# Performance work log

Measured on AMD Instinct MI355X. Metric: run time of the kernel, lower is better.

The kernel has to match this reference:

```python
import jax, jax.numpy as jnp
import numpy as np

NUM_HEADS = 16
NUM_GROUPS = 4
HIDDEN = 2048
HEAD_DIM = HIDDEN // NUM_HEADS  # 128


def setup_inputs() -> dict:
    key = jax.random.key(0)
    ks = jax.random.split(key, 9)
    B, S = 2, 2048
    kv_dim = NUM_GROUPS * HEAD_DIM
    sc_in = 1.0 / np.sqrt(HIDDEN)
    return {
        "X": jax.random.normal(ks[0], (B, S, HIDDEN), dtype=jnp.float32),
        "Wq": jax.random.normal(ks[1], (HIDDEN, HIDDEN), dtype=jnp.float32) * sc_in,
        "bq": jnp.zeros((HIDDEN,), jnp.float32),
        "Wk": jax.random.normal(ks[2], (kv_dim, HIDDEN), dtype=jnp.float32) * sc_in,
        "bk": jnp.zeros((kv_dim,), jnp.float32),
        "Wv": jax.random.normal(ks[3], (kv_dim, HIDDEN), dtype=jnp.float32) * sc_in,
        "bv": jnp.zeros((kv_dim,), jnp.float32),
        "Wo": jax.random.normal(ks[4], (HIDDEN, HIDDEN), dtype=jnp.float32) * sc_in,
        "bo": jnp.zeros((HIDDEN,), jnp.float32),
    }


def reference(X, Wq, bq, Wk, bk, Wv, bv, Wo, bo):
    B, S, D = X.shape
    H, G, hd = NUM_HEADS, NUM_GROUPS, HEAD_DIM
    rep = H // G

    q = X @ Wq.T + bq                          # (B,S,D)
    k = X @ Wk.T + bk                          # (B,S,G*hd)
    v = X @ Wv.T + bv                          # (B,S,G*hd)

    q = q.reshape(B, S, H, hd).transpose(0, 2, 1, 3)   # (B,H,S,hd)
    k = k.reshape(B, S, G, hd).transpose(0, 2, 1, 3)   # (B,G,S,hd)
    v = v.reshape(B, S, G, hd).transpose(0, 2, 1, 3)
    # GQA head expansion: each kv group serves rep query heads
    k = jnp.repeat(k, rep, axis=1)             # (B,H,S,hd)
    v = jnp.repeat(v, rep, axis=1)

    scale = 1.0 / jnp.sqrt(jnp.asarray(hd, X.dtype))
    scores = jnp.einsum('bhqd,bhkd->bhqk', q, k) * scale  # (B,H,S,S)
    attn = jax.nn.softmax(scores, axis=-1)
    mid = jnp.einsum('bhqk,bhkd->bhqd', attn, v)          # (B,H,S,hd)
    mid = mid.transpose(0, 2, 1, 3).reshape(B, S, D)
    return mid @ Wo.T + bo
```

## Files before the change

### kernel.cpp

```cpp
#include <hip/hip_runtime.h>

using uint = unsigned int;
using ushort = unsigned short;

typedef float f32x4 __attribute__((ext_vector_type(4)));
typedef float f32x16 __attribute__((ext_vector_type(16)));
typedef uint u32x4 __attribute__((ext_vector_type(4)));
using short8 = __attribute__((ext_vector_type(8))) short;

__device__ __forceinline__ ushort f2bf(float f) {
  uint u = __float_as_uint(f);
  u += 0x7fffu + ((u >> 16) & 1u);
  return (ushort)(u >> 16);
}

#define GLOAD_LDS16(gptr, lptr)                                                   \
  __builtin_amdgcn_global_load_lds(                                               \
      (const __attribute__((address_space(1))) void*)(gptr),                      \
      (__attribute__((address_space(3))) void*)(lptr), 16, 0, 0)

__global__ void cast_f32_to_bf16(const float* __restrict__ in,
                                 ushort* __restrict__ out, int n4) {
  int stride = gridDim.x * blockDim.x;
  for (int i = blockIdx.x * blockDim.x + threadIdx.x; i < n4; i += stride) {
    float4 v = reinterpret_cast<const float4*>(in)[i];
    ushort4 o;
    o.x = f2bf(v.x); o.y = f2bf(v.y); o.z = f2bf(v.z); o.w = f2bf(v.w);
    reinterpret_cast<ushort4*>(out)[i] = o;
  }
}

__device__ __forceinline__ void gemm128_mainloop(const ushort* __restrict__ A,
                                                 const ushort* __restrict__ W,
                                                 int K, ushort* As, ushort* Bs,
                                                 f32x4 (&acc)[4][4]) {
  const int tid = threadIdx.x;
  const int lane = tid & 63;
  const int wr = (tid >> 7) & 1;
  const int wc = (tid >> 6) & 1;
  const char* aP = (const char*)(A + (size_t)(tid >> 2) * K) + (tid & 3) * 16;
  const char* bP = (const char*)(W + (size_t)(tid >> 2) * K) + (tid & 3) * 16;
  const size_t rowHop = (size_t)64 * K * 2;
  ushort* aL0 = As + tid * 8;
  ushort* aL1 = As + 2048 + tid * 8;
  ushort* bL0 = Bs + tid * 8;
  ushort* bL1 = Bs + 2048 + tid * 8;
  const int ar = lane & 15;
  const int ak = (lane >> 4) * 8;

  for (int k0 = 0; k0 < K; k0 += 32) {
    GLOAD_LDS16(aP, aL0);
    GLOAD_LDS16(aP + rowHop, aL1);
    GLOAD_LDS16(bP, bL0);
    GLOAD_LDS16(bP + rowHop, bL1);
    aP += 64; bP += 64;
    __syncthreads();
    short8 af[4], bf[4];
#pragma unroll
    for (int i = 0; i < 4; ++i)
      af[i] = *reinterpret_cast<const short8*>(&As[(wr * 64 + i * 16 + ar) * 32 + ak]);
#pragma unroll
    for (int i = 0; i < 4; ++i)
      bf[i] = *reinterpret_cast<const short8*>(&Bs[(wc * 64 + i * 16 + ar) * 32 + ak]);
#pragma unroll
    for (int mi = 0; mi < 4; ++mi)
#pragma unroll
      for (int ni = 0; ni < 4; ++ni)
        acc[mi][ni] = __builtin_amdgcn_mfma_f32_16x16x32_bf16(af[mi], bf[ni],
                                                              acc[mi][ni], 0, 0, 0);
    __syncthreads();
  }
}

__global__ __launch_bounds__(256) void qkv_gemm(
    const ushort* __restrict__ Xb, const ushort* __restrict__ Wq,
    const ushort* __restrict__ Wk, const ushort* __restrict__ Wv,
    const float* __restrict__ bq, const float* __restrict__ bk,
    const float* __restrict__ bv, ushort* __restrict__ Qb,
    ushort* __restrict__ Kb, ushort* __restrict__ Vt) {
  __shared__ ushort As[128 * 32], Bs[128 * 32];
  const int bx = blockIdx.x, by = blockIdx.y;
  const ushort* W; const float* bias; ushort* out;
  int n0, mode, ldo;
  if (bx < 16)      { W = Wq; bias = bq; out = Qb; n0 = bx * 128;        mode = 0; ldo = 2048; }
  else if (bx < 20) { W = Wk; bias = bk; out = Kb; n0 = (bx - 16) * 128; mode = 0; ldo = 512; }
  else              { W = Wv; bias = bv; out = Vt; n0 = (bx - 20) * 128; mode = 1; ldo = 0; }

  f32x4 acc[4][4] = {};
  gemm128_mainloop(Xb + (size_t)by * 128 * 2048, W + (size_t)n0 * 2048, 2048, As, Bs, acc);

  const int lane = threadIdx.x & 63;
  const int wr = (threadIdx.x >> 7) & 1, wc = (threadIdx.x >> 6) & 1;
  const int r0 = by * 128 + wr * 64 + ((lane >> 4) * 4);
  const int c0 = wc * 64 + (lane & 15);
#pragma unroll
  for (int mi = 0; mi < 4; ++mi)
#pragma unroll
    for (int ni = 0; ni < 4; ++ni) {
      const int col = c0 + ni * 16;
      const float bb = bias[n0 + col];
#pragma unroll
      for (int j = 0; j < 4; ++j) {
        const int row = r0 + mi * 16 + j;
        const float v = acc[mi][ni][j] + bb;
        if (mode == 0) {
          out[(size_t)row * ldo + n0 + col] = f2bf(v);
        } else {
          const int b = row >> 11, s = row & 2047;
          out[((size_t)(b * 512 + n0 + col) << 11) + s] = f2bf(v);
        }
      }
    }
}

__global__ __launch_bounds__(256) void out_gemm(const ushort* __restrict__ Mid,
                                                const ushort* __restrict__ Wo,
                                                const float* __restrict__ bo,
                                                float* __restrict__ Out) {
  __shared__ ushort As[128 * 32], Bs[128 * 32];
  const int bx = blockIdx.x, by = blockIdx.y;
  f32x4 acc[4][4] = {};
  gemm128_mainloop(Mid + (size_t)by * 128 * 2048, Wo + (size_t)bx * 128 * 2048,
                   2048, As, Bs, acc);
  const int lane = threadIdx.x & 63;
  const int wr = (threadIdx.x >> 7) & 1, wc = (threadIdx.x >> 6) & 1;
  const int r0 = by * 128 + wr * 64 + ((lane >> 4) * 4);
  const int c0 = bx * 128 + wc * 64 + (lane & 15);
#pragma unroll
  for (int mi = 0; mi < 4; ++mi)
#pragma unroll
    for (int ni = 0; ni < 4; ++ni) {
      const int col = c0 + ni * 16;
      const float bb = bo[col];
#pragma unroll
      for (int j = 0; j < 4; ++j)
        Out[(size_t)(r0 + mi * 16 + j) * 2048 + col] = acc[mi][ni][j] + bb;
    }
}

__global__ __launch_bounds__(256, 2) void attn_fwd(const ushort* __restrict__ Q,
                                                   const ushort* __restrict__ Kb,
                                                   const ushort* __restrict__ Vt,
                                                   ushort* __restrict__ Mid) {
  __shared__ ushort Ks[2][64 * 128];
  __shared__ ushort Vs[2][128 * 64];

  const int tid = threadIdx.x, lane = tid & 63, wave = tid >> 6;
  const int h = blockIdx.y, b = blockIdx.z, g = h >> 2;
  const int q0w = blockIdx.x * 128 + wave * 32;
  const int lq = lane & 31, hi = lane >> 5;

  const char* kbase = (const char*)Kb + ((size_t)b * 2048 * 512 + g * 128) * 2;
  const char* vbase = (const char*)Vt + ((size_t)(b * 512 + g * 128) * 2048) * 2;
  int kRow[4], kOff[4], vRow[4], vOff[4];
#pragma unroll
  for (int i = 0; i < 4; ++i) {
    const int off = (i * 256 + tid) * 16;
    const int r = off >> 8, c = off & 255;
    kRow[i] = r; kOff[i] = c ^ ((r & 7) << 4);
    const int rv = off >> 7, cv = off & 127;
    vRow[i] = rv; vOff[i] = cv ^ ((rv & 7) << 4);
  }

#pragma unroll
  for (int i = 0; i < 4; ++i) {
    GLOAD_LDS16(kbase + (size_t)kRow[i] * 1024 + kOff[i],
                (char*)Ks[0] + (i * 256 + tid) * 16);
    GLOAD_LDS16(vbase + (size_t)vRow[i] * 4096 + vOff[i],
                (char*)Vs[0] + (i * 256 + tid) * 16);
  }

  short8 qf[8];
  {
    const ushort* qp = Q + (size_t)(b * 2048 + q0w + lq) * 2048 + h * 128 + hi * 8;
#pragma unroll
    for (int dblk = 0; dblk < 8; ++dblk)
      qf[dblk] = *reinterpret_cast<const short8*>(qp + dblk * 16);
  }

  float m_s = -3.0e38f, l_s = 0.f;
  f32x16 o[4] = {};
  const float sc2 = 0.08838834764831843f * 1.44269504088896340736f;

  __syncthreads();

  for (int t = 0; t < 32; ++t) {
    const int cur = t & 1;
    if (t < 31) {
      const int kv0 = (t + 1) * 64;
#pragma unroll
      for (int i = 0; i < 4; ++i) {
        GLOAD_LDS16(kbase + (size_t)(kv0 + kRow[i]) * 1024 + kOff[i],
                    (char*)Ks[cur ^ 1] + (i * 256 + tid) * 16);
        GLOAD_LDS16(vbase + (size_t)vRow[i] * 4096 + kv0 * 2 + vOff[i],
                    (char*)Vs[cur ^ 1] + (i * 256 + tid) * 16);
      }
    }

    const char* ksb = (const char*)Ks[cur];
    f32x16 st0 = {}, st1 = {};
    const int kcol = (32 * 0 + 16 * hi);
    const int ksw = (lq & 7) << 4;
    __builtin_amdgcn_s_setprio(1);
#pragma unroll
    for (int dblk = 0; dblk < 8; ++dblk) {
      const int cb = (dblk * 32 + 16 * hi) ^ ksw;
      short8 kf0 = *reinterpret_cast<const short8*>(ksb + lq * 256 + cb);
      short8 kf1 = *reinterpret_cast<const short8*>(ksb + (32 + lq) * 256 + cb);
      st0 = __builtin_amdgcn_mfma_f32_32x32x16_bf16(kf0, qf[dblk], st0, 0, 0, 0);
      st1 = __builtin_amdgcn_mfma_f32_32x32x16_bf16(kf1, qf[dblk], st1, 0, 0, 0);
    }
    __builtin_amdgcn_s_setprio(0);
    (void)kcol;

    float pm = fmaxf(st0[0], st0[1]);
#pragma unroll
    for (int r = 2; r < 16; ++r) pm = fmaxf(pm, st0[r]);
#pragma unroll
    for (int r = 0; r < 16; ++r) pm = fmaxf(pm, st1[r]);
    pm = fmaxf(pm, __shfl_xor(pm, 32, 64));
    const float msc = pm * sc2;

    if (__any(msc > m_s + 8.f)) {
      const float mnew = fmaxf(m_s, msc);
      const float alpha = exp2f(m_s - mnew);
      m_s = mnew;
      l_s *= alpha;
#pragma unroll
      for (int r = 0; r < 16; ++r) {
        const int qr = (r & 3) + 8 * (r >> 2) + 4 * hi;
        const float ar = __shfl(alpha, qr, 64);
#pragma unroll
        for (int dblk = 0; dblk < 4; ++dblk) o[dblk][r] *= ar;
      }
    }

    float rs = 0.f;
#pragma unroll
    for (int r = 0; r < 16; ++r) {
      st0[r] = exp2f(fmaf(st0[r], sc2, -m_s));
      rs += st0[r];
    }
#pragma unroll
    for (int r = 0; r < 16; ++r) {
      st1[r] = exp2f(fmaf(st1[r], sc2, -m_s));
      rs += st1[r];
    }
    rs += __shfl_xor(rs, 32, 64);
    l_s += rs;

    short8 pa[4];
#pragma unroll
    for (int half = 0; half < 2; ++half) {
      const f32x16 pt = half ? st1 : st0;
#pragma unroll
      for (int kk = 0; kk < 2; ++kk) {
        const int Rx = kk * 8;
        uint w0, w1, w2, w3;
#pragma unroll
        for (int s2 = 0; s2 < 2; ++s2) {
          const int s = s2 * 2;
          const float x0 = pt[Rx + s],     x1 = pt[Rx + s + 1];
          const float y0 = pt[Rx + 4 + s], y1 = pt[Rx + 4 + s + 1];
          uint x, y;
          asm("v_cvt_pk_bf16_f32 %0, %1, %2" : "=v"(x) : "v"(x0), "v"(x1));
          asm("v_cvt_pk_bf16_f32 %0, %1, %2" : "=v"(y) : "v"(y0), "v"(y1));
          auto sw = __builtin_amdgcn_permlane32_swap(x, y, false, false);
          if (s2 == 0) { w0 = sw[0]; w2 = sw[1]; }
          else         { w1 = sw[0]; w3 = sw[1]; }
        }
        u32x4 wv = {w0, w1, w2, w3};
        pa[half * 2 + kk] = __builtin_bit_cast(short8, wv);
      }
    }

    const char* vsb = (const char*)Vs[cur];
    __builtin_amdgcn_s_setprio(1);
#pragma unroll
    for (int dblk = 0; dblk < 4; ++dblk) {
      const int rv = dblk * 32 + lq;
      const int vsw = (rv & 7) << 4;
#pragma unroll
      for (int ks = 0; ks < 4; ++ks) {
        short8 vf = *reinterpret_cast<const short8*>(
            vsb + rv * 128 + ((ks * 32 + 16 * hi) ^ vsw));
        o[dblk] = __builtin_amdgcn_mfma_f32_32x32x16_bf16(pa[ks], vf, o[dblk], 0, 0, 0);
      }
    }
    __builtin_amdgcn_s_setprio(0);

    __syncthreads();
  }

  const float linv = 1.f / l_s;
#pragma unroll
  for (int r = 0; r < 16; ++r) {
    const int qr = (r & 3) + 8 * (r >> 2) + 4 * hi;
    const float lv = __shfl(linv, qr, 64);
    ushort* mp = Mid + (size_t)(b * 2048 + q0w + qr) * 2048 + h * 128 + lq;
#pragma unroll
    for (int dblk = 0; dblk < 4; ++dblk)
      mp[dblk * 32] = f2bf(o[dblk][r] * lv);
  }
}

extern "C" void kernel_launch(void* const* d_in, const int* in_sizes, int n_in,
                              void* d_out, int out_size, void* d_ws, size_t ws_size,
                              hipStream_t stream) {
  const float* X  = (const float*)d_in[0];
  const float* Wq = (const float*)d_in[1];
  const float* bq = (const float*)d_in[2];
  const float* Wk = (const float*)d_in[3];
  const float* bk = (const float*)d_in[4];
  const float* Wv = (const float*)d_in[5];
  const float* bv = (const float*)d_in[6];
  const float* Wo = (const float*)d_in[7];
  const float* bo = (const float*)d_in[8];
  float* Out = (float*)d_out;

  char* ws = (char*)d_ws;
  ushort* Xb   = (ushort*)(ws);
  ushort* Wqb  = (ushort*)(ws + 16777216);
  ushort* Wkb  = (ushort*)(ws + 25165824);
  ushort* Wvb  = (ushort*)(ws + 27262976);
  ushort* Wob  = (ushort*)(ws + 29360128);
  ushort* Qb   = (ushort*)(ws + 37748736);
  ushort* Kbuf = (ushort*)(ws + 54525952);
  ushort* Vtb  = (ushort*)(ws + 58720256);
  ushort* Midb = (ushort*)(ws + 62914560);

  auto cast = [&](const float* src, ushort* dst, int n) {
    int n4 = n >> 2;
    int blocks = (n4 + 255) >> 8;
    if (blocks > 2048) blocks = 2048;
    cast_f32_to_bf16<<<dim3(blocks), dim3(256), 0, stream>>>(src, dst, n4);
  };
  cast(X,  Xb,  8388608);
  cast(Wq, Wqb, 4194304);
  cast(Wk, Wkb, 1048576);
  cast(Wv, Wvb, 1048576);
  cast(Wo, Wob, 4194304);

  qkv_gemm<<<dim3(24, 32), 256, 0, stream>>>(Xb, Wqb, Wkb, Wvb, bq, bk, bv,
                                             Qb, Kbuf, Vtb);
  attn_fwd<<<dim3(16, 16, 2), 256, 0, stream>>>(Qb, Kbuf, Vtb, Midb);
  out_gemm<<<dim3(16, 32), 256, 0, stream>>>(Midb, Wob, bo, Out);
}
```

Baseline: 227.9 us.

## Rewrite projection GEMMs as 8-wave ping-pong pipelined kernels with swizzled LDS

Replaces the 128x128 single-buffered GEMM mainloop with a templated 512-thread kernel that uses 256-wide N tiles, K=64 steps, double-buffered LDS filled by direct global-to-LDS loads with an XOR swizzle, and interleaved prefetch/MFMA phases gated by barriers and priority hints. Block IDs are remapped for L2 locality in both QKV and output GEMMs. The attention kernel's max and sum reductions become tree reductions to shorten dependency chains. The aim is to hide memory latency and cut LDS bank conflicts, at the cost of larger LDS use and fewer blocks (192 QKV blocks may underfill the GPU).

```diff
diff --git a/kernel.cpp b/kernel.cpp
--- a/kernel.cpp
+++ b/kernel.cpp
@@ -18,6 +18,8 @@
   __builtin_amdgcn_global_load_lds(                                               \
       (const __attribute__((address_space(1))) void*)(gptr),                      \
       (__attribute__((address_space(3))) void*)(lptr), 16, 0, 0)
+
+__device__ __forceinline__ int swz(int o) { return o ^ (((o >> 7) & 7) << 4); }
 
 __global__ void cast_f32_to_bf16(const float* __restrict__ in,
                                  ushort* __restrict__ out, int n4) {
@@ -30,71 +32,170 @@
   }
 }
 
-__device__ __forceinline__ void gemm128_mainloop(const ushort* __restrict__ A,
-                                                 const ushort* __restrict__ W,
-                                                 int K, ushort* As, ushort* Bs,
-                                                 f32x4 (&acc)[4][4]) {
+template <int BM>
+__device__ __forceinline__ void gemm8p(const char* Ab, const char* Bb, int K,
+                                       char* lds, f32x4 (&acc)[BM / 32][4]) {
+  constexpr int MI = BM / 32;
+  constexpr int MH = MI / 2;
+  constexpr int ABYTES = BM * 128;
+  constexpr int BUFB = ABYTES + 32768;
+  constexpr int NAU = BM / 64;
+  constexpr int TL = NAU + 4;
+
   const int tid = threadIdx.x;
   const int lane = tid & 63;
-  const int wr = (tid >> 7) & 1;
-  const int wc = (tid >> 6) & 1;
-  const char* aP = (const char*)(A + (size_t)(tid >> 2) * K) + (tid & 3) * 16;
-  const char* bP = (const char*)(W + (size_t)(tid >> 2) * K) + (tid & 3) * 16;
-  const size_t rowHop = (size_t)64 * K * 2;
-  ushort* aL0 = As + tid * 8;
-  ushort* aL1 = As + 2048 + tid * 8;
-  ushort* bL0 = Bs + tid * 8;
-  ushort* bL1 = Bs + 2048 + tid * 8;
-  const int ar = lane & 15;
-  const int ak = (lane >> 4) * 8;
-
-  for (int k0 = 0; k0 < K; k0 += 32) {
-    GLOAD_LDS16(aP, aL0);
-    GLOAD_LDS16(aP + rowHop, aL1);
-    GLOAD_LDS16(bP, bL0);
-    GLOAD_LDS16(bP + rowHop, bL1);
-    aP += 64; bP += 64;
-    __syncthreads();
-    short8 af[4], bf[4];
-#pragma unroll
-    for (int i = 0; i < 4; ++i)
-      af[i] = *reinterpret_cast<const short8*>(&As[(wr * 64 + i * 16 + ar) * 32 + ak]);
-#pragma unroll
-    for (int i = 0; i < 4; ++i)
-      bf[i] = *reinterpret_cast<const short8*>(&Bs[(wc * 64 + i * 16 + ar) * 32 + ak]);
-#pragma unroll
-    for (int mi = 0; mi < 4; ++mi)
-#pragma unroll
-      for (int ni = 0; ni < 4; ++ni)
-        acc[mi][ni] = __builtin_amdgcn_mfma_f32_16x16x32_bf16(af[mi], bf[ni],
-                                                              acc[mi][ni], 0, 0, 0);
-    __syncthreads();
-  }
-}
-
-__global__ __launch_bounds__(256) void qkv_gemm(
+  const int wm = (tid >> 8) & 1;
+  const int wn = (tid >> 6) & 3;
+  const int lr = lane & 15, lgk = lane >> 4;
+  const size_t K2 = (size_t)K * 2;
+  const int nt = K >> 6;
+
+  const char* srcA[NAU];
+#pragma unroll
+  for (int u = 0; u < NAU; ++u) {
+    int d = u * 8192 + tid * 16, s = swz(d);
+    srcA[u] = Ab + (size_t)(s >> 7) * K2 + (s & 127);
+  }
+  const char* srcB[4];
+#pragma unroll
+  for (int u = 0; u < 4; ++u) {
+    int d = u * 8192 + tid * 16, s = swz(d);
+    srcB[u] = Bb + (size_t)(s >> 7) * K2 + (s & 127);
+  }
+  char* dstA = lds + tid * 16;
+  char* dstB = lds + ABYTES + tid * 16;
+
+  auto stA = [&](int buf, int u, int t) {
+    GLOAD_LDS16(srcA[u] + (size_t)t * 128, dstA + buf * BUFB + u * 8192);
+  };
+  auto stB = [&](int buf, int u, int t) {
+    GLOAD_LDS16(srcB[u] + (size_t)t * 128, dstB + buf * BUFB + u * 8192);
+  };
+  auto rdA = [&](int buf, int mi, int kk) -> short8 {
+    int o = (wm * (BM / 2) + mi * 16 + lr) * 128 + kk * 64 + lgk * 16;
+    return *reinterpret_cast<const short8*>(lds + buf * BUFB + swz(o));
+  };
+  auto rdB = [&](int buf, int ni, int kk) -> short8 {
+    int o = (wn * 64 + ni * 16 + lr) * 128 + kk * 64 + lgk * 16;
+    return *reinterpret_cast<const short8*>(lds + buf * BUFB + ABYTES + swz(o));
+  };
+
+#pragma unroll
+  for (int u = 0; u < NAU; ++u) stA(0, u, 0);
+#pragma unroll
+  for (int u = 0; u < 4; ++u) stB(0, u, 0);
+#pragma unroll
+  for (int u = 0; u < NAU; ++u) stA(1, u, 1);
+#pragma unroll
+  for (int u = 0; u < 4; ++u) stB(1, u, 1);
+  asm volatile("s_waitcnt vmcnt(%0)" ::"n"(TL) : "memory");
+  __builtin_amdgcn_s_barrier();
+
+  short8 af[MH][2], bf[4][2];
+
+  for (int t = 0; t < nt; ++t) {
+    const int c = t & 1;
+    const bool pf = (t + 2 < nt);
+
+#pragma unroll
+    for (int mi = 0; mi < MH; ++mi) { af[mi][0] = rdA(c, mi, 0); af[mi][1] = rdA(c, mi, 1); }
+#pragma unroll
+    for (int ni = 0; ni < 2; ++ni) { bf[ni][0] = rdB(c, ni, 0); bf[ni][1] = rdB(c, ni, 1); }
+    __builtin_amdgcn_s_barrier();
+    __builtin_amdgcn_s_setprio(1);
+#pragma unroll
+    for (int mi = 0; mi < MH; ++mi)
+#pragma unroll
+      for (int ni = 0; ni < 2; ++ni)
+#pragma unroll
+        for (int kk = 0; kk < 2; ++kk)
+          acc[mi][ni] = __builtin_amdgcn_mfma_f32_16x16x32_bf16(af[mi][kk], bf[ni][kk], acc[mi][ni], 0, 0, 0);
+    __builtin_amdgcn_s_setprio(0);
+    __builtin_amdgcn_s_barrier();
+
+#pragma unroll
+    for (int ni = 2; ni < 4; ++ni) { bf[ni][0] = rdB(c, ni, 0); bf[ni][1] = rdB(c, ni, 1); }
+    if (pf) {
+      if constexpr (BM == 256) { stA(c, 0, t + 2); stA(c, 2, t + 2); }
+    }
+    __builtin_amdgcn_s_barrier();
+    __builtin_amdgcn_s_setprio(1);
+#pragma unroll
+    for (int mi = 0; mi < MH; ++mi)
+#pragma unroll
+      for (int ni = 2; ni < 4; ++ni)
+#pragma unroll
+        for (int kk = 0; kk < 2; ++kk)
+          acc[mi][ni] = __builtin_amdgcn_mfma_f32_16x16x32_bf16(af[mi][kk], bf[ni][kk], acc[mi][ni], 0, 0, 0);
+    __builtin_amdgcn_s_setprio(0);
+    __builtin_amdgcn_s_barrier();
+
+#pragma unroll
+    for (int mi = 0; mi < MH; ++mi) { af[mi][0] = rdA(c, MH + mi, 0); af[mi][1] = rdA(c, MH + mi, 1); }
+    if (pf) {
+#pragma unroll
+      for (int u = 0; u < 4; ++u) stB(c, u, t + 2);
+    }
+    __builtin_amdgcn_s_barrier();
+    __builtin_amdgcn_s_setprio(1);
+#pragma unroll
+    for (int mi = 0; mi < MH; ++mi)
+#pragma unroll
+      for (int ni = 0; ni < 2; ++ni)
+#pragma unroll
+        for (int kk = 0; kk < 2; ++kk)
+          acc[MH + mi][ni] = __builtin_amdgcn_mfma_f32_16x16x32_bf16(af[mi][kk], bf[ni][kk], acc[MH + mi][ni], 0, 0, 0);
+    __builtin_amdgcn_s_setprio(0);
+    __builtin_amdgcn_s_barrier();
+
+    if (pf) {
+      if constexpr (BM == 256) { stA(c, 1, t + 2); stA(c, 3, t + 2); }
+      else                     { stA(c, 0, t + 2); stA(c, 1, t + 2); }
+    }
+    __builtin_amdgcn_s_setprio(1);
+#pragma unroll
+    for (int mi = 0; mi < MH; ++mi)
+#pragma unroll
+      for (int ni = 2; ni < 4; ++ni)
+#pragma unroll
+        for (int kk = 0; kk < 2; ++kk)
+          acc[MH + mi][ni] = __builtin_amdgcn_mfma_f32_16x16x32_bf16(af[mi][kk], bf[ni][kk], acc[MH + mi][ni], 0, 0, 0);
+    __builtin_amdgcn_s_setprio(0);
+    if (t + 1 < nt) {
+      if (pf) { asm volatile("s_waitcnt vmcnt(%0)" ::"n"(TL) : "memory"); }
+      else    { asm volatile("s_waitcnt vmcnt(0)" ::: "memory"); }
+      __builtin_amdgcn_s_barrier();
+    }
+  }
+}
+
+__global__ __launch_bounds__(512) void qkv_gemm8(
     const ushort* __restrict__ Xb, const ushort* __restrict__ Wq,
     const ushort* __restrict__ Wk, const ushort* __restrict__ Wv,
     const float* __restrict__ bq, const float* __restrict__ bk,
     const float* __restrict__ bv, ushort* __restrict__ Qb,
     ushort* __restrict__ Kb, ushort* __restrict__ Vt) {
-  __shared__ ushort As[128 * 32], Bs[128 * 32];
-  const int bx = blockIdx.x, by = blockIdx.y;
+  __shared__ char lds[2 * (256 * 128 + 32768)];
+  int id = blockIdx.x;
+  id = (id & 7) * 24 + (id >> 3);
+  const int bx = id % 12, by = id / 12;
+
   const ushort* W; const float* bias; ushort* out;
   int n0, mode, ldo;
-  if (bx < 16)      { W = Wq; bias = bq; out = Qb; n0 = bx * 128;        mode = 0; ldo = 2048; }
-  else if (bx < 20) { W = Wk; bias = bk; out = Kb; n0 = (bx - 16) * 128; mode = 0; ldo = 512; }
-  else              { W = Wv; bias = bv; out = Vt; n0 = (bx - 20) * 128; mode = 1; ldo = 0; }
-
-  f32x4 acc[4][4] = {};
-  gemm128_mainloop(Xb + (size_t)by * 128 * 2048, W + (size_t)n0 * 2048, 2048, As, Bs, acc);
+  if (bx < 8)       { W = Wq; bias = bq; out = Qb; n0 = bx * 256;        mode = 0; ldo = 2048; }
+  else if (bx < 10) { W = Wk; bias = bk; out = Kb; n0 = (bx - 8) * 256;  mode = 0; ldo = 512; }
+  else              { W = Wv; bias = bv; out = Vt; n0 = (bx - 10) * 256; mode = 1; ldo = 0; }
+
+  f32x4 acc[8][4] = {};
+  gemm8p<256>((const char*)(Xb + (size_t)by * 256 * 2048),
+              (const char*)(W + (size_t)n0 * 2048), 2048, lds, acc);
 
   const int lane = threadIdx.x & 63;
-  const int wr = (threadIdx.x >> 7) & 1, wc = (threadIdx.x >> 6) & 1;
-  const int r0 = by * 128 + wr * 64 + ((lane >> 4) * 4);
-  const int c0 = wc * 64 + (lane & 15);
-#pragma unroll
-  for (int mi = 0; mi < 4; ++mi)
+  const int wm = (threadIdx.x >> 8) & 1, wn = (threadIdx.x >> 6) & 3;
+  const int r0 = by * 256 + wm * 128 + (lane >> 4) * 4;
+  const int c0 = wn * 64 + (lane & 15);
+#pragma unroll
+  for (int mi = 0; mi < 8; ++mi)
 #pragma unroll
     for (int ni = 0; ni < 4; ++ni) {
       const int col = c0 + ni * 16;
@@ -113,19 +214,23 @@
     }
 }
 
-__global__ __launch_bounds__(256) void out_gemm(const ushort* __restrict__ Mid,
-                                                const ushort* __restrict__ Wo,
-                                                const float* __restrict__ bo,
-                                                float* __restrict__ Out) {
-  __shared__ ushort As[128 * 32], Bs[128 * 32];
-  const int bx = blockIdx.x, by = blockIdx.y;
+__global__ __launch_bounds__(512) void out_gemm8(const ushort* __restrict__ Mid,
+                                                 const ushort* __restrict__ Wo,
+                                                 const float* __restrict__ bo,
+                                                 float* __restrict__ Out) {
+  __shared__ char lds[2 * (128 * 128 + 32768)];
+  int id = blockIdx.x;
+  id = (id & 7) * 32 + (id >> 3);
+  const int bx = id % 8, by = id / 8;
+
   f32x4 acc[4][4] = {};
-  gemm128_mainloop(Mid + (size_t)by * 128 * 2048, Wo + (size_t)bx * 128 * 2048,
-                   2048, As, Bs, acc);
+  gemm8p<128>((const char*)(Mid + (size_t)by * 128 * 2048),
+              (const char*)(Wo + (size_t)bx * 256 * 2048), 2048, lds, acc);
+
   const int lane = threadIdx.x & 63;
-  const int wr = (threadIdx.x >> 7) & 1, wc = (threadIdx.x >> 6) & 1;
-  const int r0 = by * 128 + wr * 64 + ((lane >> 4) * 4);
-  const int c0 = bx * 128 + wc * 64 + (lane & 15);
+  const int wm = (threadIdx.x >> 8) & 1, wn = (threadIdx.x >> 6) & 3;
+  const int r0 = by * 128 + wm * 64 + (lane >> 4) * 4;
+  const int c0 = bx * 256 + wn * 64 + (lane & 15);
 #pragma unroll
   for (int mi = 0; mi < 4; ++mi)
 #pragma unroll
@@ -199,7 +304,6 @@
 
     const char* ksb = (const char*)Ks[cur];
     f32x16 st0 = {}, st1 = {};
-    const int kcol = (32 * 0 + 16 * hi);
     const int ksw = (lq & 7) << 4;
     __builtin_amdgcn_s_setprio(1);
 #pragma unroll
@@ -211,14 +315,15 @@
       st1 = __builtin_amdgcn_mfma_f32_32x32x16_bf16(kf1, qf[dblk], st1, 0, 0, 0);
     }
     __builtin_amdgcn_s_setprio(0);
-    (void)kcol;
-
-    float pm = fmaxf(st0[0], st0[1]);
-#pragma unroll
-    for (int r = 2; r < 16; ++r) pm = fmaxf(pm, st0[r]);
-#pragma unroll
-    for (int r = 0; r < 16; ++r) pm = fmaxf(pm, st1[r]);
-    pm = fmaxf(pm, __shfl_xor(pm, 32, 64));
+
+    float mx[16];
+#pragma unroll
+    for (int r = 0; r < 16; ++r) mx[r] = fmaxf(st0[r], st1[r]);
+#pragma unroll
+    for (int s = 8; s >= 1; s >>= 1)
+#pragma unroll
+      for (int r = 0; r < s; ++r) mx[r] = fmaxf(mx[r], mx[r + s]);
+    float pm = fmaxf(mx[0], __shfl_xor(mx[0], 32, 64));
     const float msc = pm * sc2;
 
     if (__any(msc > m_s + 8.f)) {
@@ -235,17 +340,18 @@
       }
     }
 
-    float rs = 0.f;
+    float sm[16];
 #pragma unroll
     for (int r = 0; r < 16; ++r) {
       st0[r] = exp2f(fmaf(st0[r], sc2, -m_s));
-      rs += st0[r];
-    }
-#pragma unroll
-    for (int r = 0; r < 16; ++r) {
       st1[r] = exp2f(fmaf(st1[r], sc2, -m_s));
-      rs += st1[r];
-    }
+      sm[r] = st0[r] + st1[r];
+    }
+#pragma unroll
+    for (int s = 8; s >= 1; s >>= 1)
+#pragma unroll
+      for (int r = 0; r < s; ++r) sm[r] += sm[r + s];
+    float rs = sm[0];
     rs += __shfl_xor(rs, 32, 64);
     l_s += rs;
 
@@ -341,8 +447,8 @@
   cast(Wv, Wvb, 1048576);
   cast(Wo, Wob, 4194304);
 
-  qkv_gemm<<<dim3(24, 32), 256, 0, stream>>>(Xb, Wqb, Wkb, Wvb, bq, bk, bv,
-                                             Qb, Kbuf, Vtb);
+  qkv_gemm8<<<dim3(192), dim3(512), 0, stream>>>(Xb, Wqb, Wkb, Wvb, bq, bk, bv,
+                                                 Qb, Kbuf, Vtb);
   attn_fwd<<<dim3(16, 16, 2), 256, 0, stream>>>(Qb, Kbuf, Vtb, Midb);
-  out_gemm<<<dim3(16, 32), 256, 0, stream>>>(Midb, Wob, bo, Out);
-}
+  out_gemm8<<<dim3(256), dim3(512), 0, stream>>>(Midb, Wob, bo, Out);
+}
```

After: 236.4 us. 3.7% more time.

## Process two 32-row query sets per wave to reuse K/V LDS fragments

Applied to the files above, without the earlier changes.

Each wave now handles 64 query rows as two independent 32-row sets, so every K and V fragment read from LDS feeds two MFMAs. The grid is halved to 8 query blocks of 256 rows, and launch bounds drop to one block per CU to leave room for the doubled accumulators. The K swizzle widens to 16 rows, and the softmax max/sum reductions become tree-shaped. The cost is more VGPR pressure, lower occupancy, and only 256 blocks, which may leave CUs underused.

```diff
diff --git a/kernel.cpp b/kernel.cpp
--- a/kernel.cpp
+++ b/kernel.cpp
@@ -138,7 +138,7 @@
     }
 }
 
-__global__ __launch_bounds__(256, 2) void attn_fwd(const ushort* __restrict__ Q,
+__global__ __launch_bounds__(256, 1) void attn_fwd(const ushort* __restrict__ Q,
                                                    const ushort* __restrict__ Kb,
                                                    const ushort* __restrict__ Vt,
                                                    ushort* __restrict__ Mid) {
@@ -147,7 +147,7 @@
 
   const int tid = threadIdx.x, lane = tid & 63, wave = tid >> 6;
   const int h = blockIdx.y, b = blockIdx.z, g = h >> 2;
-  const int q0w = blockIdx.x * 128 + wave * 32;
+  const int q0w = blockIdx.x * 256 + wave * 64;
   const int lq = lane & 31, hi = lane >> 5;
 
   const char* kbase = (const char*)Kb + ((size_t)b * 2048 * 512 + g * 128) * 2;
@@ -157,7 +157,7 @@
   for (int i = 0; i < 4; ++i) {
     const int off = (i * 256 + tid) * 16;
     const int r = off >> 8, c = off & 255;
-    kRow[i] = r; kOff[i] = c ^ ((r & 7) << 4);
+    kRow[i] = r; kOff[i] = c ^ ((r & 15) << 4);
     const int rv = off >> 7, cv = off & 127;
     vRow[i] = rv; vOff[i] = cv ^ ((rv & 7) << 4);
   }
@@ -170,19 +170,24 @@
                 (char*)Vs[0] + (i * 256 + tid) * 16);
   }
 
-  short8 qf[8];
-  {
-    const ushort* qp = Q + (size_t)(b * 2048 + q0w + lq) * 2048 + h * 128 + hi * 8;
+  short8 qf[2][8];
+#pragma unroll
+  for (int set = 0; set < 2; ++set) {
+    const ushort* qp =
+        Q + (size_t)(b * 2048 + q0w + set * 32 + lq) * 2048 + h * 128 + hi * 8;
 #pragma unroll
     for (int dblk = 0; dblk < 8; ++dblk)
-      qf[dblk] = *reinterpret_cast<const short8*>(qp + dblk * 16);
-  }
-
-  float m_s = -3.0e38f, l_s = 0.f;
-  f32x16 o[4] = {};
+      qf[set][dblk] = *reinterpret_cast<const short8*>(qp + dblk * 16);
+  }
+
+  float m_s[2] = {-3.0e38f, -3.0e38f}, l_s[2] = {0.f, 0.f};
+  f32x16 o[2][4] = {};
   const float sc2 = 0.08838834764831843f * 1.44269504088896340736f;
 
   __syncthreads();
+
+  const int ksw = (lq & 15) << 4;
+  const int vsw = (lq & 7) << 4;
 
   for (int t = 0; t < 32; ++t) {
     const int cur = t & 1;
@@ -198,79 +203,87 @@
     }
 
     const char* ksb = (const char*)Ks[cur];
-    f32x16 st0 = {}, st1 = {};
-    const int kcol = (32 * 0 + 16 * hi);
-    const int ksw = (lq & 7) << 4;
+    f32x16 st[2][2] = {};
     __builtin_amdgcn_s_setprio(1);
 #pragma unroll
     for (int dblk = 0; dblk < 8; ++dblk) {
       const int cb = (dblk * 32 + 16 * hi) ^ ksw;
       short8 kf0 = *reinterpret_cast<const short8*>(ksb + lq * 256 + cb);
       short8 kf1 = *reinterpret_cast<const short8*>(ksb + (32 + lq) * 256 + cb);
-      st0 = __builtin_amdgcn_mfma_f32_32x32x16_bf16(kf0, qf[dblk], st0, 0, 0, 0);
-      st1 = __builtin_amdgcn_mfma_f32_32x32x16_bf16(kf1, qf[dblk], st1, 0, 0, 0);
+      st[0][0] = __builtin_amdgcn_mfma_f32_32x32x16_bf16(kf0, qf[0][dblk], st[0][0], 0, 0, 0);
+      st[0][1] = __builtin_amdgcn_mfma_f32_32x32x16_bf16(kf1, qf[0][dblk], st[0][1], 0, 0, 0);
+      st[1][0] = __builtin_amdgcn_mfma_f32_32x32x16_bf16(kf0, qf[1][dblk], st[1][0], 0, 0, 0);
+      st[1][1] = __builtin_amdgcn_mfma_f32_32x32x16_bf16(kf1, qf[1][dblk], st[1][1], 0, 0, 0);
     }
     __builtin_amdgcn_s_setprio(0);
-    (void)kcol;
-
-    float pm = fmaxf(st0[0], st0[1]);
-#pragma unroll
-    for (int r = 2; r < 16; ++r) pm = fmaxf(pm, st0[r]);
-#pragma unroll
-    for (int r = 0; r < 16; ++r) pm = fmaxf(pm, st1[r]);
-    pm = fmaxf(pm, __shfl_xor(pm, 32, 64));
-    const float msc = pm * sc2;
-
-    if (__any(msc > m_s + 8.f)) {
-      const float mnew = fmaxf(m_s, msc);
-      const float alpha = exp2f(m_s - mnew);
-      m_s = mnew;
-      l_s *= alpha;
-#pragma unroll
-      for (int r = 0; r < 16; ++r) {
-        const int qr = (r & 3) + 8 * (r >> 2) + 4 * hi;
-        const float ar = __shfl(alpha, qr, 64);
-#pragma unroll
-        for (int dblk = 0; dblk < 4; ++dblk) o[dblk][r] *= ar;
-      }
-    }
-
-    float rs = 0.f;
-#pragma unroll
-    for (int r = 0; r < 16; ++r) {
-      st0[r] = exp2f(fmaf(st0[r], sc2, -m_s));
-      rs += st0[r];
-    }
-#pragma unroll
-    for (int r = 0; r < 16; ++r) {
-      st1[r] = exp2f(fmaf(st1[r], sc2, -m_s));
-      rs += st1[r];
-    }
-    rs += __shfl_xor(rs, 32, 64);
-    l_s += rs;
-
-    short8 pa[4];
-#pragma unroll
-    for (int half = 0; half < 2; ++half) {
-      const f32x16 pt = half ? st1 : st0;
-#pragma unroll
-      for (int kk = 0; kk < 2; ++kk) {
-        const int Rx = kk * 8;
-        uint w0, w1, w2, w3;
-#pragma unroll
-        for (int s2 = 0; s2 < 2; ++s2) {
-          const int s = s2 * 2;
-          const float x0 = pt[Rx + s],     x1 = pt[Rx + s + 1];
-          const float y0 = pt[Rx + 4 + s], y1 = pt[Rx + 4 + s + 1];
-          uint x, y;
-          asm("v_cvt_pk_bf16_f32 %0, %1, %2" : "=v"(x) : "v"(x0), "v"(x1));
-          asm("v_cvt_pk_bf16_f32 %0, %1, %2" : "=v"(y) : "v"(y0), "v"(y1));
-          auto sw = __builtin_amdgcn_permlane32_swap(x, y, false, false);
-          if (s2 == 0) { w0 = sw[0]; w2 = sw[1]; }
-          else         { w1 = sw[0]; w3 = sw[1]; }
+
+    short8 pa[2][4];
+#pragma unroll
+    for (int set = 0; set < 2; ++set) {
+      float mx[8];
+#pragma unroll
+      for (int r = 0; r < 8; ++r)
+        mx[r] = fmaxf(fmaxf(st[set][0][r], st[set][0][r + 8]),
+                      fmaxf(st[set][1][r], st[set][1][r + 8]));
+#pragma unroll
+      for (int s = 4; s >= 1; s >>= 1)
+#pragma unroll
+        for (int r = 0; r < s; ++r) mx[r] = fmaxf(mx[r], mx[r + s]);
+      float pm = fmaxf(mx[0], __shfl_xor(mx[0], 32, 64));
+      const float msc = pm * sc2;
+
+      if (__any(msc > m_s[set] + 8.f)) {
+        const float mnew = fmaxf(m_s[set], msc);
+        const float alpha = exp2f(m_s[set] - mnew);
+        m_s[set] = mnew;
+        l_s[set] *= alpha;
+#pragma unroll
+        for (int r = 0; r < 16; ++r) {
+          const int qr = (r & 3) + 8 * (r >> 2) + 4 * hi;
+          const float ar = __shfl(alpha, qr, 64);
+#pragma unroll
+          for (int dblk = 0; dblk < 4; ++dblk) o[set][dblk][r] *= ar;
         }
-        u32x4 wv = {w0, w1, w2, w3};
-        pa[half * 2 + kk] = __builtin_bit_cast(short8, wv);
+      }
+
+      float sm[8];
+#pragma unroll
+      for (int half = 0; half < 2; ++half)
+#pragma unroll
+        for (int r = 0; r < 16; ++r)
+          st[set][half][r] = exp2f(fmaf(st[set][half][r], sc2, -m_s[set]));
+#pragma unroll
+      for (int r = 0; r < 8; ++r)
+        sm[r] = (st[set][0][r] + st[set][0][r + 8]) +
+                (st[set][1][r] + st[set][1][r + 8]);
+#pragma unroll
+      for (int s = 4; s >= 1; s >>= 1)
+#pragma unroll
+        for (int r = 0; r < s; ++r) sm[r] += sm[r + s];
+      float rs = sm[0] + __shfl_xor(sm[0], 32, 64);
+      l_s[set] += rs;
+
+#pragma unroll
+      for (int half = 0; half < 2; ++half) {
+#pragma unroll
+        for (int kk = 0; kk < 2; ++kk) {
+          const int Rx = kk * 8;
+          uint w0, w1, w2, w3;
+#pragma unroll
+          for (int s2 = 0; s2 < 2; ++s2) {
+            const int s = s2 * 2;
+            const float x0 = st[set][half][Rx + s],     x1 = st[set][half][Rx + s + 1];
+            const float y0 = st[set][half][Rx + 4 + s], y1 = st[set][half][Rx + 4 + s + 1];
+            uint x, y;
+            asm("v_cvt_pk_bf16_f32 %0, %1, %2" : "=v"(x) : "v"(x0), "v"(x1));
+            asm("v_cvt_pk_bf16_f32 %0, %1, %2" : "=v"(y) : "v"(y0), "v"(y1));
+            auto sw = __builtin_amdgcn_permlane32_swap(x, y, false, false);
+            if (s2 == 0) { w0 = sw[0]; w2 = sw[1]; }
+            else         { w1 = sw[0]; w3 = sw[1]; }
+          }
+          u32x4 wv = {w0, w1, w2, w3};
+          pa[set][half * 2 + kk] = __builtin_bit_cast(short8, wv);
+        }
       }
     }
 
@@ -279,12 +292,12 @@
 #pragma unroll
     for (int dblk = 0; dblk < 4; ++dblk) {
       const int rv = dblk * 32 + lq;
-      const int vsw = (rv & 7) << 4;
 #pragma unroll
       for (int ks = 0; ks < 4; ++ks) {
         short8 vf = *reinterpret_cast<const short8*>(
             vsb + rv * 128 + ((ks * 32 + 16 * hi) ^ vsw));
-        o[dblk] = __builtin_amdgcn_mfma_f32_32x32x16_bf16(pa[ks], vf, o[dblk], 0, 0, 0);
+        o[0][dblk] = __builtin_amdgcn_mfma_f32_32x32x16_bf16(pa[0][ks], vf, o[0][dblk], 0, 0, 0);
+        o[1][dblk] = __builtin_amdgcn_mfma_f32_32x32x16_bf16(pa[1][ks], vf, o[1][dblk], 0, 0, 0);
       }
     }
     __builtin_amdgcn_s_setprio(0);
@@ -292,15 +305,18 @@
     __syncthreads();
   }
 
-  const float linv = 1.f / l_s;
-#pragma unroll
-  for (int r = 0; r < 16; ++r) {
-    const int qr = (r & 3) + 8 * (r >> 2) + 4 * hi;
-    const float lv = __shfl(linv, qr, 64);
-    ushort* mp = Mid + (size_t)(b * 2048 + q0w + qr) * 2048 + h * 128 + lq;
-#pragma unroll
-    for (int dblk = 0; dblk < 4; ++dblk)
-      mp[dblk * 32] = f2bf(o[dblk][r] * lv);
+#pragma unroll
+  for (int set = 0; set < 2; ++set) {
+    const float linv = 1.f / l_s[set];
+#pragma unroll
+    for (int r = 0; r < 16; ++r) {
+      const int qr = (r & 3) + 8 * (r >> 2) + 4 * hi;
+      const float lv = __shfl(linv, qr, 64);
+      ushort* mp = Mid + (size_t)(b * 2048 + q0w + set * 32 + qr) * 2048 + h * 128 + lq;
+#pragma unroll
+      for (int dblk = 0; dblk < 4; ++dblk)
+        mp[dblk * 32] = f2bf(o[set][dblk][r] * lv);
+    }
   }
 }
 
@@ -343,6 +359,6 @@
 
   qkv_gemm<<<dim3(24, 32), 256, 0, stream>>>(Xb, Wqb, Wkb, Wvb, bq, bk, bv,
                                              Qb, Kbuf, Vtb);
-  attn_fwd<<<dim3(16, 16, 2), 256, 0, stream>>>(Qb, Kbuf, Vtb, Midb);
+  attn_fwd<<<dim3(8, 16, 2), 256, 0, stream>>>(Qb, Kbuf, Vtb, Midb);
   out_gemm<<<dim3(16, 32), 256, 0, stream>>>(Midb, Wob, bo, Out);
 }
```

After: 263.6 us. 1.16x slower.

## Fuse bf16 casts into one launch, widen K LDS swizzle, tree-reduce softmax stats

Applied to the files above, without the earlier changes.

Replaces five separate f32-to-bf16 cast launches with a single kernel that walks all five tensors into the contiguous workspace, removing launch overhead and tail effects. In attention, the K tile swizzle in LDS now uses 16 rows instead of 8 to spread 256-byte rows across more banks and cut read conflicts. The row max and row sum use tree reductions instead of serial chains, shortening dependency latency. The fused cast adds per-element branching to pick the source tensor.

```diff
diff --git a/kernel.cpp b/kernel.cpp
--- a/kernel.cpp
+++ b/kernel.cpp
@@ -19,14 +19,30 @@
       (const __attribute__((address_space(1))) void*)(gptr),                      \
       (__attribute__((address_space(3))) void*)(lptr), 16, 0, 0)
 
-__global__ void cast_f32_to_bf16(const float* __restrict__ in,
-                                 ushort* __restrict__ out, int n4) {
-  int stride = gridDim.x * blockDim.x;
-  for (int i = blockIdx.x * blockDim.x + threadIdx.x; i < n4; i += stride) {
-    float4 v = reinterpret_cast<const float4*>(in)[i];
+__global__ void cast_all_bf16(const float* __restrict__ X,
+                              const float* __restrict__ Wq,
+                              const float* __restrict__ Wk,
+                              const float* __restrict__ Wv,
+                              const float* __restrict__ Wo,
+                              ushort* __restrict__ dst ) {
+  const int e0 = 2097152;
+  const int e1 = e0 + 1048576;
+  const int e2 = e1 + 262144;
+  const int e3 = e2 + 262144;
+  const int e4 = e3 + 1048576;
+  const int stride = gridDim.x * blockDim.x;
+  for (int i = blockIdx.x * blockDim.x + threadIdx.x; i < e4; i += stride) {
+    const float* src;
+    int j;
+    if (i < e0)      { src = X;  j = i; }
+    else if (i < e1) { src = Wq; j = i - e0; }
+    else if (i < e2) { src = Wk; j = i - e1; }
+    else if (i < e3) { src = Wv; j = i - e2; }
+    else             { src = Wo; j = i - e3; }
+    float4 v = reinterpret_cast<const float4*>(src)[j];
     ushort4 o;
     o.x = f2bf(v.x); o.y = f2bf(v.y); o.z = f2bf(v.z); o.w = f2bf(v.w);
-    reinterpret_cast<ushort4*>(out)[i] = o;
+    reinterpret_cast<ushort4*>(dst)[i] = o;
   }
 }
 
@@ -157,7 +173,7 @@
   for (int i = 0; i < 4; ++i) {
     const int off = (i * 256 + tid) * 16;
     const int r = off >> 8, c = off & 255;
-    kRow[i] = r; kOff[i] = c ^ ((r & 7) << 4);
+    kRow[i] = r; kOff[i] = c ^ ((r & 15) << 4);
     const int rv = off >> 7, cv = off & 127;
     vRow[i] = rv; vOff[i] = cv ^ ((rv & 7) << 4);
   }
@@ -184,6 +200,8 @@
 
   __syncthreads();
 
+  const int ksw = (lq & 15) << 4;
+
   for (int t = 0; t < 32; ++t) {
     const int cur = t & 1;
     if (t < 31) {
@@ -199,8 +217,6 @@
 
     const char* ksb = (const char*)Ks[cur];
     f32x16 st0 = {}, st1 = {};
-    const int kcol = (32 * 0 + 16 * hi);
-    const int ksw = (lq & 7) << 4;
     __builtin_amdgcn_s_setprio(1);
 #pragma unroll
     for (int dblk = 0; dblk < 8; ++dblk) {
@@ -211,14 +227,15 @@
       st1 = __builtin_amdgcn_mfma_f32_32x32x16_bf16(kf1, qf[dblk], st1, 0, 0, 0);
     }
     __builtin_amdgcn_s_setprio(0);
-    (void)kcol;
-
-    float pm = fmaxf(st0[0], st0[1]);
-#pragma unroll
-    for (int r = 2; r < 16; ++r) pm = fmaxf(pm, st0[r]);
-#pragma unroll
-    for (int r = 0; r < 16; ++r) pm = fmaxf(pm, st1[r]);
-    pm = fmaxf(pm, __shfl_xor(pm, 32, 64));
+
+    float mx[16];
+#pragma unroll
+    for (int r = 0; r < 16; ++r) mx[r] = fmaxf(st0[r], st1[r]);
+#pragma unroll
+    for (int s = 8; s >= 1; s >>= 1)
+#pragma unroll
+      for (int r = 0; r < s; ++r) mx[r] = fmaxf(mx[r], mx[r + s]);
+    float pm = fmaxf(mx[0], __shfl_xor(mx[0], 32, 64));
     const float msc = pm * sc2;
 
     if (__any(msc > m_s + 8.f)) {
@@ -235,17 +252,18 @@
       }
     }
 
-    float rs = 0.f;
+    float sm[16];
 #pragma unroll
     for (int r = 0; r < 16; ++r) {
       st0[r] = exp2f(fmaf(st0[r], sc2, -m_s));
-      rs += st0[r];
-    }
-#pragma unroll
-    for (int r = 0; r < 16; ++r) {
       st1[r] = exp2f(fmaf(st1[r], sc2, -m_s));
-      rs += st1[r];
-    }
+      sm[r] = st0[r] + st1[r];
+    }
+#pragma unroll
+    for (int s = 8; s >= 1; s >>= 1)
+#pragma unroll
+      for (int r = 0; r < s; ++r) sm[r] += sm[r + s];
+    float rs = sm[0];
     rs += __shfl_xor(rs, 32, 64);
     l_s += rs;
 
@@ -279,11 +297,11 @@
 #pragma unroll
     for (int dblk = 0; dblk < 4; ++dblk) {
       const int rv = dblk * 32 + lq;
-      const int vsw = (rv & 7) << 4;
+      const int vsw2 = (rv & 7) << 4;
 #pragma unroll
       for (int ks = 0; ks < 4; ++ks) {
         short8 vf = *reinterpret_cast<const short8*>(
-            vsb + rv * 128 + ((ks * 32 + 16 * hi) ^ vsw));
+            vsb + rv * 128 + ((ks * 32 + 16 * hi) ^ vsw2));
         o[dblk] = __builtin_amdgcn_mfma_f32_32x32x16_bf16(pa[ks], vf, o[dblk], 0, 0, 0);
       }
     }
@@ -329,17 +347,7 @@
   ushort* Vtb  = (ushort*)(ws + 58720256);
   ushort* Midb = (ushort*)(ws + 62914560);
 
-  auto cast = [&](const float* src, ushort* dst, int n) {
-    int n4 = n >> 2;
-    int blocks = (n4 + 255) >> 8;
-    if (blocks > 2048) blocks = 2048;
-    cast_f32_to_bf16<<<dim3(blocks), dim3(256), 0, stream>>>(src, dst, n4);
-  };
-  cast(X,  Xb,  8388608);
-  cast(Wq, Wqb, 4194304);
-  cast(Wk, Wkb, 1048576);
-  cast(Wv, Wvb, 1048576);
-  cast(Wo, Wob, 4194304);
+  cast_all_bf16<<<dim3(2048), dim3(256), 0, stream>>>(X, Wq, Wk, Wv, Wo, Xb);
 
   qkv_gemm<<<dim3(24, 32), 256, 0, stream>>>(Xb, Wqb, Wkb, Wvb, bq, bk, bv,
                                              Qb, Kbuf, Vtb);
```

Measured after the change: 224.9 us. No clear change (-1.3%).
